# Kernel optimization log

Measured on AMD Instinct MI355X. Metric: run time of the kernel, lower is better.

Reference implementation:

```python
import jax, jax.numpy as jnp
import numpy as np
import math

B, T, C = 4, 2048, 1024
D_ATTN, N_HEAD = 1024, 16
HEAD = D_ATTN // N_HEAD


def setup_inputs() -> dict:
    key = jax.random.key(0)
    k1, k2, k3 = jax.random.split(key, 3)
    x = jax.random.normal(k1, (B, T, C), dtype=jnp.float32)
    mask = jnp.tril(jnp.ones((T, T), dtype=jnp.int32))  # causal mask, 0 = blocked
    W_qkv = jax.random.normal(k2, (C, 3 * D_ATTN), dtype=jnp.float32) * (1.0 / math.sqrt(C))
    b_qkv = jnp.zeros((3 * D_ATTN,), dtype=jnp.float32)
    W_out = jax.random.normal(k3, (D_ATTN, C), dtype=jnp.float32) * (1.0 / math.sqrt(D_ATTN))
    b_out = jnp.zeros((C,), dtype=jnp.float32)
    return {"x": x, "mask": mask, "W_qkv": W_qkv, "b_qkv": b_qkv, "W_out": W_out, "b_out": b_out}


def reference(x, mask, W_qkv, b_qkv, W_out, b_out):
    Bx, Tx, Cx = x.shape
    qkv = x @ W_qkv + b_qkv                      # [B, T, 3*d_attn]
    q, k, v = jnp.split(qkv, 3, axis=-1)
    # [B, T, d_attn] -> [B, H, T, head]
    q = q.reshape(Bx, Tx, N_HEAD, HEAD).transpose(0, 2, 1, 3)
    k = k.reshape(Bx, Tx, N_HEAD, HEAD).transpose(0, 2, 1, 3)
    v = v.reshape(Bx, Tx, N_HEAD, HEAD).transpose(0, 2, 1, 3)
    scale = 1.0 / math.sqrt(HEAD)
    scores = jnp.einsum('bhqd,bhkd->bhqk', q, k) * scale  # [B, H, T, T]
    scores = jnp.where(mask == 0, -jnp.inf, scores)
    att = jax.nn.softmax(scores, axis=-1)
    out = jnp.einsum('bhqk,bhkd->bhqd', att, v)           # [B, H, T, head]
    out = out.transpose(0, 2, 1, 3).reshape(Bx, Tx, D_ATTN)
    return out @ W_out + b_out
```

## Files before the change

kernel.cpp:

```cpp
#include <hip/hip_runtime.h>

#define B_    4
#define T_    2048
#define C_    1024
#define DATTN 1024
#define NHEAD 16
#define M_    (B_*T_)
#define NQKV  (3*DATTN)

typedef __bf16 bf16;
typedef bf16  bf16x8 __attribute__((ext_vector_type(8)));
typedef float f32x4  __attribute__((ext_vector_type(4)));
typedef unsigned short u16x8 __attribute__((ext_vector_type(8)));

#define NEGBIG (-1e30f)

typedef const __attribute__((address_space(1))) unsigned int* gas_u32;
typedef __attribute__((address_space(3))) unsigned int* las_u32;

__global__ void detect_dtype(const unsigned short* __restrict__ x, int* flag) {
    __shared__ int cnt;
    if (threadIdx.x == 0) cnt = 0;
    __syncthreads();
    int local = 0;
    for (int j = 0; j < 8; ++j) {
        u16x8 v = *(const u16x8*)&x[(j * 256 + threadIdx.x) * 8];
        for (int k = 0; k < 8; ++k)
            if ((v[k] & 0x7F80) == 0x7F80) ++local;
    }
    atomicAdd(&cnt, local);
    __syncthreads();
    if (threadIdx.x == 0) *flag = (cnt > 0) ? 1 : 0;
}

__global__ void convert_x_any(const void* __restrict__ src, bf16* __restrict__ dst,
                              int n, const int* __restrict__ flag) {
    int i = (blockIdx.x * 256 + threadIdx.x) * 8;
    if (i >= n) return;
    if (*flag == 0) {
        *(bf16x8*)&dst[i] = *(const bf16x8*)((const bf16*)src + i);
    } else {
        const float* s = (const float*)src + i;
        f32x4 a = *(const f32x4*)s, b2 = *(const f32x4*)(s + 4);
        bf16x8 r;
        r[0] = (bf16)a[0]; r[1] = (bf16)a[1]; r[2] = (bf16)a[2]; r[3] = (bf16)a[3];
        r[4] = (bf16)b2[0]; r[5] = (bf16)b2[1]; r[6] = (bf16)b2[2]; r[7] = (bf16)b2[3];
        *(bf16x8*)&dst[i] = r;
    }
}

__global__ void prep_bias(const void* __restrict__ bq, const void* __restrict__ bo,
                          bf16* __restrict__ dq, bf16* __restrict__ do_,
                          const int* __restrict__ flag) {
    const int f = *flag;
    int i = blockIdx.x * 256 + threadIdx.x;
    if (i < NQKV)
        dq[i] = f ? (bf16)((const float*)bq)[i] : ((const bf16*)bq)[i];
    else if (i - NQKV < C_)
        do_[i - NQKV] = f ? (bf16)((const float*)bo)[i - NQKV] : ((const bf16*)bo)[i - NQKV];
}

__global__ void transpose_w_any(const void* __restrict__ src, bf16* __restrict__ dst,
                                int R, int C, const int* __restrict__ flag) {
    __shared__ bf16 tile[32][33];
    const int f = *flag;
    const int c0 = blockIdx.x * 32, r0 = blockIdx.y * 32;
    const int tx = threadIdx.x & 31, ty = threadIdx.x >> 5;
    for (int p = 0; p < 4; ++p) {
        int row = p * 8 + ty;
        size_t idx = (size_t)(r0 + row) * C + c0 + tx;
        float v = f ? ((const float*)src)[idx] : (float)((const bf16*)src)[idx];
        tile[row][tx] = (bf16)v;
    }
    __syncthreads();
    for (int p = 0; p < 4; ++p) {
        int row = p * 8 + ty;
        dst[(size_t)(c0 + row) * R + r0 + tx] = tile[tx][row];
    }
}

__global__ void transpose_v(const bf16* __restrict__ qkv, bf16* __restrict__ vt) {
    __shared__ bf16 tile[32][33];
    const int t0 = blockIdx.x * 32, d0 = blockIdx.y * 32, bh = blockIdx.z;
    const int b = bh >> 4, h = bh & 15;
    const int tx = threadIdx.x & 31, ty = threadIdx.x >> 5;
    for (int p = 0; p < 4; ++p) {
        int tt = p * 8 + ty;
        tile[tt][tx] = qkv[((size_t)b * T_ + t0 + tt) * NQKV + 2 * DATTN + h * 64 + d0 + tx];
    }
    __syncthreads();
    for (int p = 0; p < 4; ++p) {
        int dd = p * 8 + ty;
        vt[((size_t)bh * 64 + d0 + dd) * T_ + t0 + tx] = tile[tx][dd];
    }
}

template<typename TC>
__global__ __launch_bounds__(256) void gemm_bt(const bf16* __restrict__ A,
                                               const bf16* __restrict__ Bt,
                                               const bf16* __restrict__ bias,
                                               TC* __restrict__ Cc,
                                               int M, int N, int K,
                                               const int* __restrict__ flag, int want) {
    if (flag && *flag != want) return;
    __shared__ __align__(16) bf16 As[128 * 64];
    __shared__ __align__(16) bf16 Bs[128 * 64];
    const int tid  = threadIdx.x;
    const int lane = tid & 63, wave = tid >> 6;
    const int quad = lane >> 4, l15 = lane & 15;
    const int wr = wave >> 1, wc = wave & 1;
    const int m0 = blockIdx.y * 128, n0 = blockIdx.x * 128;
    const int srow = lane >> 3;
    const int scol = ((lane & 7) ^ srow) * 8;
    const int l7x8 = (l15 & 7);

    f32x4 acc[4][4];
    for (int i = 0; i < 4; ++i)
        for (int j = 0; j < 4; ++j)
            acc[i][j] = f32x4{0.f, 0.f, 0.f, 0.f};

    for (int k0 = 0; k0 < K; k0 += 64) {
        for (int c = 0; c < 4; ++c) {
            int chunk = wave * 4 + c;
            int row = chunk * 8 + srow;
            __builtin_amdgcn_global_load_lds(
                (gas_u32)&A[(size_t)(m0 + row) * K + k0 + scol],
                (las_u32)&As[chunk * 512], 16, 0, 0);
            __builtin_amdgcn_global_load_lds(
                (gas_u32)&Bt[(size_t)(n0 + row) * K + k0 + scol],
                (las_u32)&Bs[chunk * 512], 16, 0, 0);
        }
        __syncthreads();
        for (int ks = 0; ks < 2; ++ks) {
            bf16x8 af[4], bfr[4];
            for (int i = 0; i < 4; ++i)
                af[i] = *(const bf16x8*)&As[(wr * 64 + i * 16 + l15) * 64 +
                                            (((ks * 4 + quad) ^ l7x8) * 8)];
            for (int j = 0; j < 4; ++j)
                bfr[j] = *(const bf16x8*)&Bs[(wc * 64 + j * 16 + l15) * 64 +
                                             (((ks * 4 + quad) ^ l7x8) * 8)];
            for (int i = 0; i < 4; ++i)
                for (int j = 0; j < 4; ++j)
                    acc[i][j] = __builtin_amdgcn_mfma_f32_16x16x32_bf16(af[i], bfr[j], acc[i][j], 0, 0, 0);
        }
        __syncthreads();
    }

    for (int i = 0; i < 4; ++i) {
        int row = m0 + wr * 64 + i * 16 + quad * 4;
        for (int j = 0; j < 4; ++j) {
            int col = n0 + wc * 64 + j * 16 + l15;
            float bv = (float)bias[col];
            for (int r = 0; r < 4; ++r) {
                float v = acc[i][j][r] + bv;
                if constexpr (__is_same(TC, float)) Cc[(size_t)(row + r) * N + col] = v;
                else                                Cc[(size_t)(row + r) * N + col] = (bf16)v;
            }
        }
    }
}

__global__ __launch_bounds__(256) void attn_fused6(const bf16* __restrict__ qkv,
                                                   const bf16* __restrict__ vt,
                                                   bf16* __restrict__ out) {
    __shared__ __align__(16) bf16 Ks[2][64 * 64];
    __shared__ __align__(16) bf16 Vs[2][64 * 64];
    __shared__ __align__(16) bf16 Ps[2 * 4 * 16 * 72];
    const int tid  = threadIdx.x;
    const int lane = tid & 63, wave = tid >> 6;
    const int quad = lane >> 4, l15 = lane & 15;
    const int srow = lane >> 3;
    const int scol = ((lane & 7) ^ srow) * 8;
    const int l7x8 = (l15 & 7);
    const int bh = blockIdx.x & 63;
    const int i  = blockIdx.x >> 6;
    const int b  = bh >> 4, h = bh & 15;
    const int lo = i, hi = 31 - i;
    const size_t rowbase = (size_t)b * T_;
    const float SC = 0.125f * 1.44269504088896f;

    auto stage = [&](int kt, int buf) {
        const int k0 = kt * 64;
        for (int p = 0; p < 2; ++p) {
            int chunk = wave * 2 + p;
            int row = chunk * 8 + srow;
            __builtin_amdgcn_global_load_lds(
                (gas_u32)&qkv[(rowbase + k0 + row) * NQKV + DATTN + h * 64 + scol],
                (las_u32)&Ks[buf][chunk * 512], 16, 0, 0);
            __builtin_amdgcn_global_load_lds(
                (gas_u32)&vt[((size_t)bh * 64 + row) * T_ + k0 + scol],
                (las_u32)&Vs[buf][chunk * 512], 16, 0, 0);
        }
    };

    bf16x8 qf[2][2];
#pragma unroll
    for (int t = 0; t < 2; ++t) {
        int q0 = (t ? hi : lo) * 64;
        size_t r = rowbase + q0 + wave * 16 + l15;
        const bf16* p = &qkv[r * NQKV + h * 64];
        qf[t][0] = *(const bf16x8*)&p[quad * 8];
        qf[t][1] = *(const bf16x8*)&p[32 + quad * 8];
    }

    f32x4 oa[2][4];
    float lacc[2][4];
#pragma unroll
    for (int t = 0; t < 2; ++t)
        for (int c = 0; c < 4; ++c) {
            oa[t][c] = f32x4{0.f, 0.f, 0.f, 0.f};
            lacc[t][c] = 0.f;
        }

    bf16* Pw0 = &Ps[(0 * 4 + wave) * 16 * 72];
    bf16* Pw1 = &Ps[(1 * 4 + wave) * 16 * 72];

    stage(0, 0);

    for (int kt = 0; kt <= hi; ++kt) {
        const int k0 = kt * 64;
        const bool act0 = (kt <= lo);
        const int buf = kt & 1;
        __syncthreads();
        if (kt < hi) stage(kt + 1, buf ^ 1);

        const bf16* Kb = Ks[buf];
        const bf16* Vb = Vs[buf];

        f32x4 s0[4], s1[4];
        for (int c = 0; c < 4; ++c) {
            s0[c] = f32x4{0.f, 0.f, 0.f, 0.f};
            s1[c] = f32x4{0.f, 0.f, 0.f, 0.f};
        }
        for (int ks = 0; ks < 2; ++ks)
            for (int c = 0; c < 4; ++c) {
                bf16x8 kf = *(const bf16x8*)&Kb[(c * 16 + l15) * 64 +
                                                (((ks * 4 + quad) ^ l7x8) * 8)];
                if (act0) s0[c] = __builtin_amdgcn_mfma_f32_16x16x32_bf16(qf[0][ks], kf, s0[c], 0, 0, 0);
                s1[c] = __builtin_amdgcn_mfma_f32_16x16x32_bf16(qf[1][ks], kf, s1[c], 0, 0, 0);
            }

#pragma unroll
        for (int t = 0; t < 2; ++t) {
            if (t == 0 && !act0) continue;
            const int q0 = (t ? hi : lo) * 64;
            const bool diag = (kt == (t ? hi : lo));
            bf16* Pw = t ? Pw1 : Pw0;
            for (int c = 0; c < 4; ++c) {
                int key = k0 + c * 16 + l15;
                for (int r = 0; r < 4; ++r) {
                    float v = (t ? s1[c][r] : s0[c][r]) * SC;
                    if (diag && key > q0 + wave * 16 + quad * 4 + r) v = NEGBIG;
                    float p = __builtin_amdgcn_exp2f(v);
                    lacc[t][r] += p;
                    Pw[(quad * 4 + r) * 72 + c * 16 + l15] = (bf16)p;
                }
            }
        }

        for (int ks2 = 0; ks2 < 2; ++ks2) {
            bf16x8 pf0{}, pf1;
            if (act0) pf0 = *(const bf16x8*)&Pw0[l15 * 72 + ks2 * 32 + quad * 8];
            pf1 = *(const bf16x8*)&Pw1[l15 * 72 + ks2 * 32 + quad * 8];
            for (int c2 = 0; c2 < 4; ++c2) {
                bf16x8 vf = *(const bf16x8*)&Vb[(c2 * 16 + l15) * 64 +
                                                (((ks2 * 4 + quad) ^ l7x8) * 8)];
                if (act0) oa[0][c2] = __builtin_amdgcn_mfma_f32_16x16x32_bf16(pf0, vf, oa[0][c2], 0, 0, 0);
                oa[1][c2] = __builtin_amdgcn_mfma_f32_16x16x32_bf16(pf1, vf, oa[1][c2], 0, 0, 0);
            }
        }
    }

#pragma unroll
    for (int t = 0; t < 2; ++t) {
        int q0 = (t ? hi : lo) * 64;
        float inv[4];
        for (int r = 0; r < 4; ++r) {
            float v = lacc[t][r];
            for (int off = 1; off < 16; off <<= 1) v += __shfl_xor(v, off);
            inv[r] = 1.f / v;
        }
        size_t r0 = rowbase + q0 + wave * 16 + quad * 4;
        for (int c2 = 0; c2 < 4; ++c2) {
            int col = h * 64 + c2 * 16 + l15;
            for (int r = 0; r < 4; ++r)
                out[(r0 + r) * (size_t)DATTN + col] = (bf16)(oa[t][c2][r] * inv[r]);
        }
    }
}

extern "C" void kernel_launch(void* const* d_in, const int* in_sizes, int n_in,
                              void* d_out, int out_size, void* d_ws, size_t ws_size,
                              hipStream_t stream) {
    const void* x     = d_in[0];
    const void* W_qkv = d_in[2];
    const void* b_qkv = d_in[3];
    const void* W_out = d_in[4];
    const void* b_out = d_in[5];

    char* ws = (char*)d_ws;
    int*  flag    = (int*)ws;
    bf16* qkv_buf = (bf16*)(ws + 256);
    bf16* Wqkv_t  = (bf16*)(ws + 256 + 50331648);
    bf16* Wout_t  = (bf16*)(ws + 256 + 56623104);
    bf16* att_buf = (bf16*)(ws + 256 + 58720256);
    bf16* vt_buf  = (bf16*)(ws + 256 + 75497472);
    bf16* x_bf    = (bf16*)(ws + 256 + 92274688);
    bf16* bq_bf   = (bf16*)(ws + 256 + 109051904);
    bf16* bo_bf   = (bf16*)(ws + 256 + 109058048);

    detect_dtype<<<1, 256, 0, stream>>>((const unsigned short*)x, flag);

    convert_x_any<<<M_ * C_ / (256 * 8), 256, 0, stream>>>(x, x_bf, M_ * C_, flag);
    prep_bias<<<(NQKV + C_) / 256, 256, 0, stream>>>(b_qkv, b_out, bq_bf, bo_bf, flag);
    transpose_w_any<<<dim3(NQKV / 32, C_ / 32), 256, 0, stream>>>(W_qkv, Wqkv_t, C_, NQKV, flag);
    transpose_w_any<<<dim3(C_ / 32, DATTN / 32), 256, 0, stream>>>(W_out, Wout_t, DATTN, C_, flag);

    gemm_bt<bf16><<<dim3(NQKV / 128, M_ / 128), 256, 0, stream>>>(
        x_bf, Wqkv_t, bq_bf, qkv_buf, M_, NQKV, C_, nullptr, 0);

    transpose_v<<<dim3(T_ / 32, 2, B_ * NHEAD), 256, 0, stream>>>(qkv_buf, vt_buf);

    attn_fused6<<<dim3(B_ * NHEAD * 16), 256, 0, stream>>>(qkv_buf, vt_buf, att_buf);

    gemm_bt<bf16 ><<<dim3(C_ / 128, M_ / 128), 256, 0, stream>>>(
        att_buf, Wout_t, bo_bf, (bf16*)d_out, M_, C_, DATTN, flag, 0);
    gemm_bt<float><<<dim3(C_ / 128, M_ / 128), 256, 0, stream>>>(
        att_buf, Wout_t, bo_bf, (float*)d_out, M_, C_, DATTN, flag, 1);
}
```

Baseline: 306.3 us.

## Transpose attention MFMAs, pack P into swizzled LDS, fold Q scale and XCD-aware GEMM tiling

The attention kernel now computes S^T and O^T by swapping the MFMA operands. Each lane then holds four consecutive keys for one query, so P is packed into bf16 pairs and written to an XOR-swizzled LDS buffer with 8-byte stores, and the row sum reduces across only two shuffles. The softmax scale is folded into the Q columns in the QKV GEMM epilogue, which removes a multiply per score. The GEMMs switch to a 1D grid remapped so consecutive row tiles land on the same XCD for L2 reuse. Output stores become vectorized 4-wide. Risks include the bf16 rounding of pre-scaled Q differing slightly from the reference, and the unconditional pf0 read of Pp[0] when act0 is false, which is harmless only because the result is unused.

```diff
diff --git a/kernel.cpp b/kernel.cpp
--- a/kernel.cpp
+++ b/kernel.cpp
@@ -10,13 +10,21 @@
 
 typedef __bf16 bf16;
 typedef bf16  bf16x8 __attribute__((ext_vector_type(8)));
+typedef bf16  bf16x4 __attribute__((ext_vector_type(4)));
 typedef float f32x4  __attribute__((ext_vector_type(4)));
 typedef unsigned short u16x8 __attribute__((ext_vector_type(8)));
 
 #define NEGBIG (-1e30f)
+#define QSCALE (0.125f * 1.44269504088896f)
 
 typedef const __attribute__((address_space(1))) unsigned int* gas_u32;
 typedef __attribute__((address_space(3))) unsigned int* las_u32;
+
+static __device__ __forceinline__ unsigned pack_bf16(float lo, float hi) {
+    unsigned short l = __builtin_bit_cast(unsigned short, (bf16)lo);
+    unsigned short h = __builtin_bit_cast(unsigned short, (bf16)hi);
+    return ((unsigned)h << 16) | l;
+}
 
 __global__ void detect_dtype(const unsigned short* __restrict__ x, int* flag) {
     __shared__ int cnt;
@@ -100,7 +108,8 @@
                                                const bf16* __restrict__ Bt,
                                                const bf16* __restrict__ bias,
                                                TC* __restrict__ Cc,
-                                               int M, int N, int K,
+                                               int N, int K, int nx,
+                                               int qn, float qs,
                                                const int* __restrict__ flag, int want) {
     if (flag && *flag != want) return;
     __shared__ __align__(16) bf16 As[128 * 64];
@@ -109,7 +118,10 @@
     const int lane = tid & 63, wave = tid >> 6;
     const int quad = lane >> 4, l15 = lane & 15;
     const int wr = wave >> 1, wc = wave & 1;
-    const int m0 = blockIdx.y * 128, n0 = blockIdx.x * 128;
+    const int id = blockIdx.x;
+    const int xcd = id & 7, j0 = id >> 3;
+    const int m0 = ((j0 / nx) * 8 + xcd) * 128;
+    const int n0 = (j0 % nx) * 128;
     const int srow = lane >> 3;
     const int scol = ((lane & 7) ^ srow) * 8;
     const int l7x8 = (l15 & 7);
@@ -151,8 +163,9 @@
         for (int j = 0; j < 4; ++j) {
             int col = n0 + wc * 64 + j * 16 + l15;
             float bv = (float)bias[col];
+            float sc = (col < qn) ? qs : 1.f;
             for (int r = 0; r < 4; ++r) {
-                float v = acc[i][j][r] + bv;
+                float v = (acc[i][j][r] + bv) * sc;
                 if constexpr (__is_same(TC, float)) Cc[(size_t)(row + r) * N + col] = v;
                 else                                Cc[(size_t)(row + r) * N + col] = (bf16)v;
             }
@@ -160,24 +173,23 @@
     }
 }
 
-__global__ __launch_bounds__(256) void attn_fused6(const bf16* __restrict__ qkv,
+__global__ __launch_bounds__(256) void attn_fused7(const bf16* __restrict__ qkv,
                                                    const bf16* __restrict__ vt,
                                                    bf16* __restrict__ out) {
     __shared__ __align__(16) bf16 Ks[2][64 * 64];
     __shared__ __align__(16) bf16 Vs[2][64 * 64];
-    __shared__ __align__(16) bf16 Ps[2 * 4 * 16 * 72];
+    __shared__ __align__(16) unsigned Pp[2][4][16 * 32];
     const int tid  = threadIdx.x;
     const int lane = tid & 63, wave = tid >> 6;
     const int quad = lane >> 4, l15 = lane & 15;
+    const int l7 = l15 & 7;
     const int srow = lane >> 3;
     const int scol = ((lane & 7) ^ srow) * 8;
-    const int l7x8 = (l15 & 7);
     const int bh = blockIdx.x & 63;
     const int i  = blockIdx.x >> 6;
     const int b  = bh >> 4, h = bh & 15;
     const int lo = i, hi = 31 - i;
     const size_t rowbase = (size_t)b * T_;
-    const float SC = 0.125f * 1.44269504088896f;
 
     auto stage = [&](int kt, int buf) {
         const int k0 = kt * 64;
@@ -204,16 +216,11 @@
     }
 
     f32x4 oa[2][4];
-    float lacc[2][4];
+    float lacc[2] = {0.f, 0.f};
 #pragma unroll
     for (int t = 0; t < 2; ++t)
-        for (int c = 0; c < 4; ++c) {
+        for (int c = 0; c < 4; ++c)
             oa[t][c] = f32x4{0.f, 0.f, 0.f, 0.f};
-            lacc[t][c] = 0.f;
-        }
-
-    bf16* Pw0 = &Ps[(0 * 4 + wave) * 16 * 72];
-    bf16* Pw1 = &Ps[(1 * 4 + wave) * 16 * 72];
 
     stage(0, 0);
 
@@ -235,9 +242,9 @@
         for (int ks = 0; ks < 2; ++ks)
             for (int c = 0; c < 4; ++c) {
                 bf16x8 kf = *(const bf16x8*)&Kb[(c * 16 + l15) * 64 +
-                                                (((ks * 4 + quad) ^ l7x8) * 8)];
-                if (act0) s0[c] = __builtin_amdgcn_mfma_f32_16x16x32_bf16(qf[0][ks], kf, s0[c], 0, 0, 0);
-                s1[c] = __builtin_amdgcn_mfma_f32_16x16x32_bf16(qf[1][ks], kf, s1[c], 0, 0, 0);
+                                                (((ks * 4 + quad) ^ l7) * 8)];
+                if (act0) s0[c] = __builtin_amdgcn_mfma_f32_16x16x32_bf16(kf, qf[0][ks], s0[c], 0, 0, 0);
+                s1[c] = __builtin_amdgcn_mfma_f32_16x16x32_bf16(kf, qf[1][ks], s1[c], 0, 0, 0);
             }
 
 #pragma unroll
@@ -245,28 +252,35 @@
             if (t == 0 && !act0) continue;
             const int q0 = (t ? hi : lo) * 64;
             const bool diag = (kt == (t ? hi : lo));
-            bf16* Pw = t ? Pw1 : Pw0;
+            const int q = q0 + wave * 16 + l15;
+            unsigned* Pw = &Pp[t][wave][0];
+            float lsum = 0.f;
             for (int c = 0; c < 4; ++c) {
-                int key = k0 + c * 16 + l15;
+                int keyb = k0 + c * 16 + quad * 4;
+                float e[4];
                 for (int r = 0; r < 4; ++r) {
-                    float v = (t ? s1[c][r] : s0[c][r]) * SC;
-                    if (diag && key > q0 + wave * 16 + quad * 4 + r) v = NEGBIG;
-                    float p = __builtin_amdgcn_exp2f(v);
-                    lacc[t][r] += p;
-                    Pw[(quad * 4 + r) * 72 + c * 16 + l15] = (bf16)p;
+                    float v = t ? s1[c][r] : s0[c][r];
+                    if (diag && keyb + r > q) v = NEGBIG;
+                    e[r] = __builtin_amdgcn_exp2f(v);
+                    lsum += e[r];
                 }
+                int g = c * 2 + (quad >> 1);
+                int wbase = l15 * 32 + (((g ^ l7) << 2) | ((quad & 1) * 2));
+                uint2 u; u.x = pack_bf16(e[0], e[1]); u.y = pack_bf16(e[2], e[3]);
+                *(uint2*)&Pw[wbase] = u;
             }
+            lacc[t] += lsum;
         }
 
         for (int ks2 = 0; ks2 < 2; ++ks2) {
-            bf16x8 pf0{}, pf1;
-            if (act0) pf0 = *(const bf16x8*)&Pw0[l15 * 72 + ks2 * 32 + quad * 8];
-            pf1 = *(const bf16x8*)&Pw1[l15 * 72 + ks2 * 32 + quad * 8];
+            int rbase = l15 * 32 + (((ks2 * 4 + quad) ^ l7) << 2);
+            bf16x8 pf0 = *(const bf16x8*)&Pp[0][wave][rbase];
+            bf16x8 pf1 = *(const bf16x8*)&Pp[1][wave][rbase];
             for (int c2 = 0; c2 < 4; ++c2) {
                 bf16x8 vf = *(const bf16x8*)&Vb[(c2 * 16 + l15) * 64 +
-                                                (((ks2 * 4 + quad) ^ l7x8) * 8)];
-                if (act0) oa[0][c2] = __builtin_amdgcn_mfma_f32_16x16x32_bf16(pf0, vf, oa[0][c2], 0, 0, 0);
-                oa[1][c2] = __builtin_amdgcn_mfma_f32_16x16x32_bf16(pf1, vf, oa[1][c2], 0, 0, 0);
+                                                (((ks2 * 4 + quad) ^ l7) * 8)];
+                if (act0) oa[0][c2] = __builtin_amdgcn_mfma_f32_16x16x32_bf16(vf, pf0, oa[0][c2], 0, 0, 0);
+                oa[1][c2] = __builtin_amdgcn_mfma_f32_16x16x32_bf16(vf, pf1, oa[1][c2], 0, 0, 0);
             }
         }
     }
@@ -274,17 +288,15 @@
 #pragma unroll
     for (int t = 0; t < 2; ++t) {
         int q0 = (t ? hi : lo) * 64;
-        float inv[4];
-        for (int r = 0; r < 4; ++r) {
-            float v = lacc[t][r];
-            for (int off = 1; off < 16; off <<= 1) v += __shfl_xor(v, off);
-            inv[r] = 1.f / v;
-        }
-        size_t r0 = rowbase + q0 + wave * 16 + quad * 4;
+        float v = lacc[t];
+        v += __shfl_xor(v, 16);
+        v += __shfl_xor(v, 32);
+        float inv = 1.f / v;
+        bf16* po = &out[(rowbase + q0 + wave * 16 + l15) * (size_t)DATTN + h * 64];
         for (int c2 = 0; c2 < 4; ++c2) {
-            int col = h * 64 + c2 * 16 + l15;
-            for (int r = 0; r < 4; ++r)
-                out[(r0 + r) * (size_t)DATTN + col] = (bf16)(oa[t][c2][r] * inv[r]);
+            bf16x4 w;
+            for (int r = 0; r < 4; ++r) w[r] = (bf16)(oa[t][c2][r] * inv);
+            *(bf16x4*)&po[c2 * 16 + quad * 4] = w;
         }
     }
 }
@@ -316,15 +328,15 @@
     transpose_w_any<<<dim3(NQKV / 32, C_ / 32), 256, 0, stream>>>(W_qkv, Wqkv_t, C_, NQKV, flag);
     transpose_w_any<<<dim3(C_ / 32, DATTN / 32), 256, 0, stream>>>(W_out, Wout_t, DATTN, C_, flag);
 
-    gemm_bt<bf16><<<dim3(NQKV / 128, M_ / 128), 256, 0, stream>>>(
-        x_bf, Wqkv_t, bq_bf, qkv_buf, M_, NQKV, C_, nullptr, 0);
+    gemm_bt<bf16><<<(NQKV / 128) * (M_ / 128), 256, 0, stream>>>(
+        x_bf, Wqkv_t, bq_bf, qkv_buf, NQKV, C_, NQKV / 128, DATTN, QSCALE, nullptr, 0);
 
     transpose_v<<<dim3(T_ / 32, 2, B_ * NHEAD), 256, 0, stream>>>(qkv_buf, vt_buf);
 
-    attn_fused6<<<dim3(B_ * NHEAD * 16), 256, 0, stream>>>(qkv_buf, vt_buf, att_buf);
-
-    gemm_bt<bf16 ><<<dim3(C_ / 128, M_ / 128), 256, 0, stream>>>(
-        att_buf, Wout_t, bo_bf, (bf16*)d_out, M_, C_, DATTN, flag, 0);
-    gemm_bt<float><<<dim3(C_ / 128, M_ / 128), 256, 0, stream>>>(
-        att_buf, Wout_t, bo_bf, (float*)d_out, M_, C_, DATTN, flag, 1);
-}
+    attn_fused7<<<dim3(B_ * NHEAD * 16), 256, 0, stream>>>(qkv_buf, vt_buf, att_buf);
+
+    gemm_bt<bf16 ><<<(C_ / 128) * (M_ / 128), 256, 0, stream>>>(
+        att_buf, Wout_t, bo_bf, (bf16*)d_out, C_, DATTN, C_ / 128, 0, 1.f, flag, 0);
+    gemm_bt<float><<<(C_ / 128) * (M_ / 128), 256, 0, stream>>>(
+        att_buf, Wout_t, bo_bf, (float*)d_out, C_, DATTN, C_ / 128, 0, 1.f, flag, 1);
+}
```

Result: no change. 311.2 us (+1.6%).
